# Optimization experiments

Measured on AMD Instinct MI355X. Metric: run time of the kernel, lower is better.

## Reference

```python
import jax, jax.numpy as jnp
import numpy as np

N_NODES = 50000
N_EDGES = 800000
IN_DIM = 128
HID_DIM = 64
N_HEADS = 4
OUT_DIM = 128
NEG_SLOPE = 0.2  # DGL GATConv default


def gat_conv(x, src, dst, W, attn_l, attn_r, bias, n_nodes):
    """DGL GATConv forward. x:[N,Fin], W:[Fin,H*D], attn_*:[H,D], bias:[H,D]. Returns [N,H,D]."""
    H, D = attn_l.shape
    h = (x @ W).reshape(n_nodes, H, D)              # [N,H,D]
    el = jnp.sum(h * attn_l[None], axis=-1)          # [N,H]
    er = jnp.sum(h * attn_r[None], axis=-1)          # [N,H]
    e = jax.nn.leaky_relu(el[src] + er[dst], NEG_SLOPE)  # [E,H]
    # edge softmax over incoming edges of each dst node (stable)
    m = jax.ops.segment_max(e, dst, num_segments=n_nodes)   # [N,H], -inf for empty
    ex = jnp.exp(e - m[dst])                                 # [E,H]
    denom = jax.ops.segment_sum(ex, dst, num_segments=n_nodes)  # [N,H]
    alpha = ex / denom[dst]                                  # [E,H]
    out = jax.ops.segment_sum(alpha[:, :, None] * h[src], dst, num_segments=n_nodes)
    return out + bias[None]                                  # [N,H,D]


def setup_inputs() -> dict:
    key = jax.random.key(0)
    ks = jax.random.split(key, 12)
    x = jax.random.normal(ks[0], (N_NODES, IN_DIM), dtype=jnp.float32)
    src = jax.random.randint(ks[1], (N_EDGES,), 0, N_NODES, dtype=jnp.int32)
    dst = jax.random.randint(ks[2], (N_EDGES,), 0, N_NODES, dtype=jnp.int32)
    s1 = 1.0 / np.sqrt(IN_DIM)
    s2 = 1.0 / np.sqrt(HID_DIM * N_HEADS)
    W1 = jax.random.normal(ks[3], (IN_DIM, N_HEADS * HID_DIM), dtype=jnp.float32) * s1
    al1 = jax.random.normal(ks[4], (N_HEADS, HID_DIM), dtype=jnp.float32) * 0.1
    ar1 = jax.random.normal(ks[5], (N_HEADS, HID_DIM), dtype=jnp.float32) * 0.1
    b1 = jnp.zeros((N_HEADS, HID_DIM), dtype=jnp.float32)
    W2 = jax.random.normal(ks[6], (N_HEADS * HID_DIM, OUT_DIM), dtype=jnp.float32) * s2
    al2 = jax.random.normal(ks[7], (1, OUT_DIM), dtype=jnp.float32) * 0.1
    ar2 = jax.random.normal(ks[8], (1, OUT_DIM), dtype=jnp.float32) * 0.1
    b2 = jnp.zeros((1, OUT_DIM), dtype=jnp.float32)
    return {"x": x, "src": src, "dst": dst, "W1": W1, "al1": al1, "ar1": ar1,
            "b1": b1, "W2": W2, "al2": al2, "ar2": ar2, "b2": b2}


def reference(x, src, dst, W1, al1, ar1, b1, W2, al2, ar2, b2):
    n = x.shape[0]
    h1 = gat_conv(x, src, dst, W1, al1, ar1, b1, n)          # [N,H,D]
    h1 = jax.nn.relu(h1).reshape(n, -1)                       # [N,H*D]
    h2 = gat_conv(h1, src, dst, W2, al2, ar2, b2, n)          # [N,1,OUT]
    return h2.reshape(n, -1)                                   # [N,OUT]
```

## Files before the change

kernel.cpp:

```cpp
#include <hip/hip_runtime.h>
#include <hip/hip_bf16.h>
#include <math.h>


#define NEG_SLOPE 0.2f
#define NB 256
#define CH 8192

typedef short short8 __attribute__((ext_vector_type(8)));
typedef float float4v __attribute__((ext_vector_type(4)));
typedef float float2v __attribute__((ext_vector_type(2)));

static __device__ __forceinline__ float lrelu(float v) {
    return v > 0.f ? v : NEG_SLOPE * v;
}

static __device__ __forceinline__ unsigned short f2bf(float f) {
    unsigned int u = __float_as_uint(f);
    u = (u + 0x7fffu + ((u >> 16) & 1u)) >> 16;
    return (unsigned short)u;
}
static __device__ __forceinline__ float bf2f(unsigned int lo16) {
    return __uint_as_float(lo16 << 16);
}

static __device__ __forceinline__ int bucket_of(int d, unsigned int M) {
    return (int)(((unsigned long long)(unsigned int)d * M) >> 32);
}

static __device__ __forceinline__ void pk_step(float2v& a00, float2v& a01,
                                               float2v& a10, float2v& a11,
                                               float2v& d0, float2v& d1,
                                               float4 w, unsigned int v) {
    float2v w01; w01[0] = w.x; w01[1] = w.y;
    float2v w23; w23[0] = w.z; w23[1] = w.w;
    float x0 = __uint_as_float(v << 16);
    float x1 = __uint_as_float(v & 0xffff0000u);
    float2v xx0 = {x0, x0};
    float2v xx1 = {x1, x1};
    asm("v_pk_fma_f32 %0, %1, %2, %0" : "+v"(a00) : "v"(w01), "v"(xx0));
    asm("v_pk_fma_f32 %0, %1, %2, %0" : "+v"(a01) : "v"(w23), "v"(xx0));
    asm("v_pk_fma_f32 %0, %1, %2, %0" : "+v"(a10) : "v"(w01), "v"(xx1));
    asm("v_pk_fma_f32 %0, %1, %2, %0" : "+v"(a11) : "v"(w23), "v"(xx1));
    asm("v_pk_add_f32 %0, %1, %0" : "+v"(d0) : "v"(w01));
    asm("v_pk_add_f32 %0, %1, %0" : "+v"(d1) : "v"(w23));
}


__global__ __launch_bounds__(256) void histbin_kernel(
        const int* __restrict__ dst, int* __restrict__ bcnt,
        int E, unsigned int M, int nblk,
        const float* __restrict__ W1, const float* __restrict__ al1,
        const float* __restrict__ ar1, const float* __restrict__ W2,
        const float* __restrict__ al2, const float* __restrict__ ar2,
        unsigned short* __restrict__ W1th, unsigned short* __restrict__ Qt1,
        unsigned short* __restrict__ Qt2, unsigned short* __restrict__ W2t) {
    int b = blockIdx.x;
    int tid = threadIdx.x;
    if (b < nblk) {
        __shared__ int lcnt[NB];
        lcnt[tid] = 0;
        __syncthreads();
        int e0 = b * CH;
        for (int i = tid; i < CH; i += 256) {
            int e = e0 + i;
            if (e < E) atomicAdd(&lcnt[bucket_of(dst[e], M)], 1);
        }
        __syncthreads();
        bcnt[b * NB + tid] = lcnt[tid];
        return;
    }
    int idx = (b - nblk) * 256 + tid;
    if (idx < 32768) {
        int h = idx >> 13;
        int r = idx & 8191;
        int d = r >> 7, k = r & 127;
        W1th[idx] = f2bf(W1[k * 256 + h * 64 + d]);
    } else if (idx < 34816) {
        int j = idx - 32768;
        int c = j >> 7, k = j & 127;
        float s = 0.f;
        if (c < 8) {
            int h = c & 3;
            const float* av = ((c < 4) ? al1 : ar1) + h * 64;
            const float* wrow = W1 + k * 256 + h * 64;
            #pragma unroll 8
            for (int d = 0; d < 64; ++d) s += wrow[d] * av[d];
        }
        Qt1[j] = f2bf(s);
    } else if (idx < 36864) {
        int j = idx - 34816;
        int c = j >> 7, k = j & 127;
        float s = (c == 0) ? al2[k] : (c == 1) ? ar2[k] : 0.f;
        Qt2[j] = f2bf(s);
    } else if (idx < 69632) {
        int j = idx - 36864;
        int m = j >> 8, k = j & 255;
        W2t[(size_t)m * 256 + k] = f2bf(W2[(size_t)k * 128 + m]);
    }
}


__global__ __launch_bounds__(256) void binscan_kernel(
        const int* __restrict__ bcnt, int* __restrict__ cur0,
        int* __restrict__ bucketStart, int nblk, int E) {
    __shared__ int s[NB];
    int t = threadIdx.x;
    int tot = 0;
    for (int blk = 0; blk < nblk; ++blk) tot += bcnt[blk * NB + t];
    s[t] = tot;
    __syncthreads();
    for (int off = 1; off < NB; off <<= 1) {
        int add = (t >= off) ? s[t - off] : 0;
        __syncthreads();
        s[t] += add;
        __syncthreads();
    }
    const int bs = s[t] - tot;
    bucketStart[t] = bs;
    if (t == NB - 1) bucketStart[NB] = E;
    int run = bs;
    for (int blk = 0; blk < nblk; ++blk) {
        int c = bcnt[blk * NB + t];
        cur0[blk * NB + t] = run;
        run += c;
    }
}


__global__ __launch_bounds__(256) void scatxdots_kernel(
        const int* __restrict__ src, const int* __restrict__ dst,
        const int* __restrict__ cur0,
        uint2* __restrict__ pairs, int E, unsigned int M, int nblk,
        const float* __restrict__ x, const unsigned short* __restrict__ Qt,
        unsigned short* __restrict__ xb,
        float* __restrict__ el, float* __restrict__ er, int N) {
    constexpr int KP = 136;
    __shared__ alignas(16) unsigned char smem[(64 + 16) * KP * 2];
    const int tid = threadIdx.x;
    if (blockIdx.x < (unsigned)nblk) {
        int* cur = (int*)smem;
        const int b = blockIdx.x;
        cur[tid] = cur0[b * NB + tid];
        __syncthreads();
        int e0 = b * CH;
        for (int i = tid; i < CH; i += 256) {
            int e = e0 + i;
            if (e < E) {
                int d = dst[e];
                int bk = bucket_of(d, M);
                int pos = atomicAdd(&cur[bk], 1);
                pairs[pos] = make_uint2((unsigned int)src[e], (unsigned int)d);
            }
        }
        return;
    }
    unsigned short* As = (unsigned short*)smem;
    unsigned short* Bs = As + 64 * KP;
    const int wid = tid >> 6, lane = tid & 63;
    const int r0 = (blockIdx.x - nblk) * 64;
    for (int ch = tid; ch < 64 * 16; ch += 256) {
        int row = ch >> 4, kc = ch & 15;
        int gr = r0 + row;
        short8 v = {};
        if (gr < N) {
            float4 a = *(const float4*)(x + (size_t)gr * 128 + kc * 8);
            float4 b = *(const float4*)(x + (size_t)gr * 128 + kc * 8 + 4);
            v[0] = (short)f2bf(a.x); v[1] = (short)f2bf(a.y);
            v[2] = (short)f2bf(a.z); v[3] = (short)f2bf(a.w);
            v[4] = (short)f2bf(b.x); v[5] = (short)f2bf(b.y);
            v[6] = (short)f2bf(b.z); v[7] = (short)f2bf(b.w);
            *(short8*)(xb + (size_t)gr * 128 + kc * 8) = v;
        }
        *(short8*)(As + row * KP + kc * 8) = v;
    }
    {
        int row = tid >> 4, kc = tid & 15;
        *(short8*)(Bs + row * KP + kc * 8) = *(const short8*)(Qt + row * 128 + kc * 8);
    }
    __syncthreads();
    float4v acc = (float4v){0.f, 0.f, 0.f, 0.f};
    const int lr = lane & 15, lk = (lane >> 4) * 8;
    #pragma unroll
    for (int ks = 0; ks < 128; ks += 32) {
        short8 af = *(const short8*)(As + (wid * 16 + lr) * KP + ks + lk);
        short8 bf_ = *(const short8*)(Bs + lr * KP + ks + lk);
        acc = __builtin_amdgcn_mfma_f32_16x16x32_bf16(af, bf_, acc, 0, 0, 0);
    }
    const int rbase = r0 + wid * 16 + (lane >> 4) * 4;
    #pragma unroll
    for (int j = 0; j < 4; ++j) {
        int row = rbase + j;
        if (row < N) {
            if (lr < 4) el[(size_t)row * 4 + lr] = acc[j];
            else if (lr < 8) er[(size_t)row * 4 + (lr - 4)] = acc[j];
        }
    }
}


__global__ __launch_bounds__(256) void bucketcsr_kernel(
        const uint2* __restrict__ pairs, const int* __restrict__ bucketStart,
        int* __restrict__ row_start, int* __restrict__ srcs,
        int N, int npb, int E) {
    __shared__ int cnt[NB];
    __shared__ int sc[NB];
    int b = blockIdx.x;
    int tid = threadIdx.x;
    int nb0 = b * npb;
    int es = bucketStart[b], ee = bucketStart[b + 1];
    cnt[tid] = 0;
    __syncthreads();
    for (int i = es + tid; i < ee; i += 256) {
        uint2 p = pairs[i];
        atomicAdd(&cnt[(int)p.y - nb0], 1);
    }
    __syncthreads();
    int myc = cnt[tid];
    sc[tid] = myc;
    __syncthreads();
    for (int off = 1; off < NB; off <<= 1) {
        int add = (tid >= off) ? sc[tid - off] : 0;
        __syncthreads();
        sc[tid] += add;
        __syncthreads();
    }
    int excl = sc[tid] - myc;
    int n = nb0 + tid;
    if (n < N && tid < npb) row_start[n] = es + excl;
    if (b == gridDim.x - 1 && tid == 0) row_start[N] = E;
    cnt[tid] = es + excl;
    __syncthreads();
    for (int i = es + tid; i < ee; i += 256) {
        uint2 p = pairs[i];
        int pos = atomicAdd(&cnt[(int)p.y - nb0], 1);
        srcs[pos] = (int)p.x;
    }
}


__global__ __launch_bounds__(256) void agg1x_kernel(const unsigned short* __restrict__ xb,
                            const float* __restrict__ el, const float* __restrict__ er,
                            const int* __restrict__ srcs, const int* __restrict__ row_start,
                            unsigned short* __restrict__ A1, int N) {
    __shared__ int   s_tbl[4][64];
    __shared__ float a_tbl[4][64][4];
    const int wslot = threadIdx.x >> 6;
    const int lane = threadIdx.x & 63;
    const int n = (blockIdx.x * 256 + threadIdx.x) >> 6;
    if (n >= N) return;
    const int rs = row_start[n];
    const int re = row_start[n + 1];

    float2v accP[2][2];
    accP[0][0] = (float2v){0.f, 0.f}; accP[0][1] = (float2v){0.f, 0.f};
    accP[1][0] = (float2v){0.f, 0.f}; accP[1][1] = (float2v){0.f, 0.f};
    float2v dP[2];
    dP[0] = (float2v){0.f, 0.f}; dP[1] = (float2v){0.f, 0.f};

    if (re > rs) {
        const float4 ern = *(const float4*)(er + (size_t)n * 4);
        for (int base = rs; base < re; base += 64) {
            const int cnt = (re - base) < 64 ? (re - base) : 64;
            asm volatile("s_waitcnt lgkmcnt(0)" ::: "memory");
            if (lane < cnt) {
                int sv = srcs[base + lane];
                float4 ev = *(const float4*)(el + (size_t)sv * 4);
                float4 av;
                av.x = __expf(lrelu(ev.x + ern.x));
                av.y = __expf(lrelu(ev.y + ern.y));
                av.z = __expf(lrelu(ev.z + ern.z));
                av.w = __expf(lrelu(ev.w + ern.w));
                s_tbl[wslot][lane] = sv;
                *(float4*)&a_tbl[wslot][lane][0] = av;
            }
            asm volatile("s_waitcnt lgkmcnt(0)" ::: "memory");
            int i = 0;
            for (; i + 4 <= cnt; i += 4) {
                int s0 = s_tbl[wslot][i],     s1 = s_tbl[wslot][i + 1];
                int s2 = s_tbl[wslot][i + 2], s3 = s_tbl[wslot][i + 3];
                float4 w0 = *(const float4*)&a_tbl[wslot][i][0];
                float4 w1 = *(const float4*)&a_tbl[wslot][i + 1][0];
                float4 w2 = *(const float4*)&a_tbl[wslot][i + 2][0];
                float4 w3 = *(const float4*)&a_tbl[wslot][i + 3][0];
                unsigned int v0 = *(const unsigned int*)(xb + (size_t)s0 * 128 + lane * 2);
                unsigned int v1 = *(const unsigned int*)(xb + (size_t)s1 * 128 + lane * 2);
                unsigned int v2 = *(const unsigned int*)(xb + (size_t)s2 * 128 + lane * 2);
                unsigned int v3 = *(const unsigned int*)(xb + (size_t)s3 * 128 + lane * 2);
                pk_step(accP[0][0], accP[0][1], accP[1][0], accP[1][1], dP[0], dP[1], w0, v0);
                pk_step(accP[0][0], accP[0][1], accP[1][0], accP[1][1], dP[0], dP[1], w1, v1);
                pk_step(accP[0][0], accP[0][1], accP[1][0], accP[1][1], dP[0], dP[1], w2, v2);
                pk_step(accP[0][0], accP[0][1], accP[1][0], accP[1][1], dP[0], dP[1], w3, v3);
            }
            for (; i < cnt; ++i) {
                int s0 = s_tbl[wslot][i];
                float4 w = *(const float4*)&a_tbl[wslot][i][0];
                unsigned int v = *(const unsigned int*)(xb + (size_t)s0 * 128 + lane * 2);
                pk_step(accP[0][0], accP[0][1], accP[1][0], accP[1][1], dP[0], dP[1], w, v);
            }
        }
        float i0 = 1.f / dP[0][0], i1 = 1.f / dP[0][1];
        float i2 = 1.f / dP[1][0], i3 = 1.f / dP[1][1];
        accP[0][0][0] *= i0; accP[1][0][0] *= i0;
        accP[0][0][1] *= i1; accP[1][0][1] *= i1;
        accP[0][1][0] *= i2; accP[1][1][0] *= i2;
        accP[0][1][1] *= i3; accP[1][1][1] *= i3;
    }
    unsigned int pk;
    pk = (unsigned int)f2bf(accP[0][0][0]) | ((unsigned int)f2bf(accP[1][0][0]) << 16);
    *(unsigned int*)(A1 + (size_t)n * 512 + 0 * 128 + lane * 2) = pk;
    pk = (unsigned int)f2bf(accP[0][0][1]) | ((unsigned int)f2bf(accP[1][0][1]) << 16);
    *(unsigned int*)(A1 + (size_t)n * 512 + 1 * 128 + lane * 2) = pk;
    pk = (unsigned int)f2bf(accP[0][1][0]) | ((unsigned int)f2bf(accP[1][1][0]) << 16);
    *(unsigned int*)(A1 + (size_t)n * 512 + 2 * 128 + lane * 2) = pk;
    pk = (unsigned int)f2bf(accP[0][1][1]) | ((unsigned int)f2bf(accP[1][1][1]) << 16);
    *(unsigned int*)(A1 + (size_t)n * 512 + 3 * 128 + lane * 2) = pk;
}


__global__ __launch_bounds__(256) void l2fused_kernel(
        const unsigned short* __restrict__ A1,
        const unsigned short* __restrict__ W1th,
        const float* __restrict__ b1,
        const unsigned short* __restrict__ W2t,
        const unsigned short* __restrict__ Qt2,
        unsigned short* __restrict__ h2b,
        float* __restrict__ el2, float* __restrict__ er2,
        int N) {
    constexpr int KP = 136;
    constexpr int PP = 72;
    __shared__ unsigned short As[64 * KP];
    __shared__ unsigned short Bs1[64 * KP];
    __shared__ unsigned short Bs2[128 * PP];
    __shared__ unsigned short Ps[64 * PP];
    __shared__ unsigned short Qs[16 * KP];
    const int tid = threadIdx.x;
    const int wid = tid >> 6, lane = tid & 63;
    const int lr = lane & 15, lk = (lane >> 4) * 8;
    const int r0 = blockIdx.x * 64;

    {
        int row = tid >> 4, kc = tid & 15;
        *(short8*)(Qs + row * KP + kc * 8) = *(const short8*)(Qt2 + row * 128 + kc * 8);
    }

    float4v acc2[8];
    #pragma unroll
    for (int cf = 0; cf < 8; ++cf) acc2[cf] = (float4v){0.f, 0.f, 0.f, 0.f};

    for (int h = 0; h < 4; ++h) {
        __syncthreads();
        for (int ch = tid; ch < 1024; ch += 256) {
            int row = ch >> 4, kc = ch & 15;
            int gr = r0 + row;
            short8 v = {};
            if (gr < N) v = *(const short8*)(A1 + (size_t)gr * 512 + h * 128 + kc * 8);
            *(short8*)(As + row * KP + kc * 8) = v;
        }
        for (int ch = tid; ch < 1024; ch += 256) {
            int row = ch >> 4, kc = ch & 15;
            *(short8*)(Bs1 + row * KP + kc * 8) =
                *(const short8*)(W1th + (size_t)h * 8192 + row * 128 + kc * 8);
        }
        for (int ch = tid; ch < 1024; ch += 256) {
            int m = ch >> 3, kc = ch & 7;
            *(short8*)(Bs2 + m * PP + kc * 8) =
                *(const short8*)(W2t + (size_t)m * 256 + h * 64 + kc * 8);
        }
        __syncthreads();

        float4v p[4];
        #pragma unroll
        for (int cf = 0; cf < 4; ++cf) p[cf] = (float4v){0.f, 0.f, 0.f, 0.f};
        #pragma unroll
        for (int ks = 0; ks < 128; ks += 32) {
            short8 af = *(const short8*)(As + (wid * 16 + lr) * KP + ks + lk);
            #pragma unroll
            for (int cf = 0; cf < 4; ++cf) {
                short8 bfr = *(const short8*)(Bs1 + (cf * 16 + lr) * KP + ks + lk);
                p[cf] = __builtin_amdgcn_mfma_f32_16x16x32_bf16(af, bfr, p[cf], 0, 0, 0);
            }
        }
        const int prow = wid * 16 + (lane >> 4) * 4;
        #pragma unroll
        for (int cf = 0; cf < 4; ++cf) {
            float bias = b1[h * 64 + cf * 16 + lr];
            #pragma unroll
            for (int j = 0; j < 4; ++j)
                Ps[(prow + j) * PP + cf * 16 + lr] = f2bf(fmaxf(p[cf][j] + bias, 0.f));
        }
        __syncthreads();

        #pragma unroll
        for (int ks2 = 0; ks2 < 64; ks2 += 32) {
            short8 af2 = *(const short8*)(Ps + (wid * 16 + lr) * PP + ks2 + lk);
            #pragma unroll
            for (int cf = 0; cf < 8; ++cf) {
                short8 bf2 = *(const short8*)(Bs2 + (cf * 16 + lr) * PP + ks2 + lk);
                acc2[cf] = __builtin_amdgcn_mfma_f32_16x16x32_bf16(af2, bf2, acc2[cf], 0, 0, 0);
            }
        }
    }

    const int prow = wid * 16 + (lane >> 4) * 4;
    #pragma unroll
    for (int cf = 0; cf < 8; ++cf) {
        int col = cf * 16 + lr;
        #pragma unroll
        for (int j = 0; j < 4; ++j) {
            unsigned short hv = f2bf(acc2[cf][j]);
            int row = prow + j;
            if (r0 + row < N) h2b[(size_t)(r0 + row) * 128 + col] = hv;
            As[row * KP + col] = hv;
        }
    }
    __syncthreads();
    float4v dd = (float4v){0.f, 0.f, 0.f, 0.f};
    #pragma unroll
    for (int ks = 0; ks < 128; ks += 32) {
        short8 af = *(const short8*)(As + (wid * 16 + lr) * KP + ks + lk);
        short8 bq = *(const short8*)(Qs + lr * KP + ks + lk);
        dd = __builtin_amdgcn_mfma_f32_16x16x32_bf16(af, bq, dd, 0, 0, 0);
    }
    #pragma unroll
    for (int j = 0; j < 4; ++j) {
        int row = r0 + prow + j;
        if (row < N) {
            if (lr == 0) el2[row] = dd[j];
            else if (lr == 1) er2[row] = dd[j];
        }
    }
}


__global__ __launch_bounds__(256) void agg2_kernel(const unsigned short* __restrict__ hb,
                           const float* __restrict__ el, const float* __restrict__ er,
                           const int* __restrict__ srcs, const int* __restrict__ row_start,
                           const float* __restrict__ bias, float* __restrict__ out, int N) {
    __shared__ uint2 t_tbl[4][64];
    const int wslot = threadIdx.x >> 6;
    const int lane = threadIdx.x & 63;
    const int n = (blockIdx.x * 256 + threadIdx.x) >> 6;
    if (n >= N) return;
    const int rs = row_start[n];
    const int re = row_start[n + 1];

    float acc0 = 0.f, acc1 = 0.f, d = 0.f;

    if (re > rs) {
        const float ern = er[n];
        for (int base = rs; base < re; base += 64) {
            const int cnt = (re - base) < 64 ? (re - base) : 64;
            asm volatile("s_waitcnt lgkmcnt(0)" ::: "memory");
            if (lane < cnt) {
                int sv = srcs[base + lane];
                float a = __expf(lrelu(el[sv] + ern));
                t_tbl[wslot][lane] = make_uint2((unsigned int)sv, __float_as_uint(a));
            }
            asm volatile("s_waitcnt lgkmcnt(0)" ::: "memory");
            int i = 0;
            for (; i + 4 <= cnt; i += 4) {
                uint2 t0 = t_tbl[wslot][i],     t1 = t_tbl[wslot][i + 1];
                uint2 t2 = t_tbl[wslot][i + 2], t3 = t_tbl[wslot][i + 3];
                float w0 = __uint_as_float(t0.y), w1 = __uint_as_float(t1.y);
                float w2 = __uint_as_float(t2.y), w3 = __uint_as_float(t3.y);
                unsigned int v0 = *(const unsigned int*)(hb + (size_t)t0.x * 128 + lane * 2);
                unsigned int v1 = *(const unsigned int*)(hb + (size_t)t1.x * 128 + lane * 2);
                unsigned int v2 = *(const unsigned int*)(hb + (size_t)t2.x * 128 + lane * 2);
                unsigned int v3 = *(const unsigned int*)(hb + (size_t)t3.x * 128 + lane * 2);
                d += w0 + w1 + w2 + w3;
                acc0 += w0 * bf2f(v0 & 0xffffu) + w1 * bf2f(v1 & 0xffffu) +
                        w2 * bf2f(v2 & 0xffffu) + w3 * bf2f(v3 & 0xffffu);
                acc1 += w0 * bf2f(v0 >> 16) + w1 * bf2f(v1 >> 16) +
                        w2 * bf2f(v2 >> 16) + w3 * bf2f(v3 >> 16);
            }
            for (; i < cnt; ++i) {
                uint2 t = t_tbl[wslot][i];
                float w = __uint_as_float(t.y);
                unsigned int v = *(const unsigned int*)(hb + (size_t)t.x * 128 + lane * 2);
                d += w;
                acc0 += w * bf2f(v & 0xffffu);
                acc1 += w * bf2f(v >> 16);
            }
        }
        float invd = 1.f / d;
        acc0 *= invd; acc1 *= invd;
    }
    float o0 = acc0 + bias[lane * 2];
    float o1 = acc1 + bias[lane * 2 + 1];
    *(float2*)(out + (size_t)n * 128 + lane * 2) = make_float2(o0, o1);
}


extern "C" void kernel_launch(void* const* d_in, const int* in_sizes, int n_in,
                              void* d_out, int out_size, void* d_ws, size_t ws_size,
                              hipStream_t stream) {
    const float* x   = (const float*)d_in[0];
    const int*   src = (const int*)d_in[1];
    const int*   dst = (const int*)d_in[2];
    const float* W1  = (const float*)d_in[3];
    const float* al1 = (const float*)d_in[4];
    const float* ar1 = (const float*)d_in[5];
    const float* b1  = (const float*)d_in[6];
    const float* W2  = (const float*)d_in[7];
    const float* al2 = (const float*)d_in[8];
    const float* ar2 = (const float*)d_in[9];
    const float* b2  = (const float*)d_in[10];
    float* out = (float*)d_out;

    const int N = in_sizes[0] / 128;
    const int E = in_sizes[1];
    const int npb = (N + NB - 1) / NB;
    const unsigned int M =
        (unsigned int)(((1ULL << 32) + npb - 1) / (unsigned long long)npb);
    const int nblk_e = (E + CH - 1) / CH;

    char* ws = (char*)d_ws;
    size_t oXB   = 0;
    size_t oA1   = oXB + (size_t)N * 128 * 2;
    size_t oH2   = oA1 + (size_t)N * 512 * 2;
    size_t oW1th = oH2 + (size_t)N * 128 * 2;
    size_t oQt1  = oW1th + 32768 * 2;
    size_t oQt2  = oQt1 + 2048 * 2;
    size_t oW2t  = oQt2 + 2048 * 2;
    size_t oEl1  = oW2t + 32768 * 2;
    size_t oEr1  = oEl1 + (size_t)N * 4 * 4;
    size_t oEl2  = oEr1 + (size_t)N * 4 * 4;
    size_t oEr2  = oEl2 + (size_t)N * 4;
    size_t oRow  = oEr2 + (size_t)N * 4;
    size_t oBcnt = oRow + (((size_t)(N + 1) * 4 + 15) & ~(size_t)15);
    size_t oCur0 = oBcnt + (size_t)nblk_e * NB * 4;
    size_t oBkS  = oCur0 + (size_t)nblk_e * NB * 4;
    size_t oPair = (oBkS + (NB + 1) * 4 + 15) & ~(size_t)15;
    size_t oSrcs = oPair + (size_t)E * 8;

    unsigned short* xb   = (unsigned short*)(ws + oXB);
    unsigned short* A1   = (unsigned short*)(ws + oA1);
    unsigned short* h2b  = (unsigned short*)(ws + oH2);
    unsigned short* w1th = (unsigned short*)(ws + oW1th);
    unsigned short* qt1  = (unsigned short*)(ws + oQt1);
    unsigned short* qt2  = (unsigned short*)(ws + oQt2);
    unsigned short* w2t  = (unsigned short*)(ws + oW2t);
    float* el1 = (float*)(ws + oEl1);
    float* er1 = (float*)(ws + oEr1);
    float* el2 = (float*)(ws + oEl2);
    float* er2 = (float*)(ws + oEr2);
    int*   row_start   = (int*)(ws + oRow);
    int*   bcnt        = (int*)(ws + oBcnt);
    int*   cur0        = (int*)(ws + oCur0);
    int*   bucketStart = (int*)(ws + oBkS);
    uint2* pairs       = (uint2*)(ws + oPair);
    int*   srcs        = (int*)(ws + oSrcs);

    const int nrowb = (N + 63) / 64;
    const int nwaveb = (N + 3) / 4;

    histbin_kernel<<<nblk_e + 272, 256, 0, stream>>>(
        dst, bcnt, E, M, nblk_e, W1, al1, ar1, W2, al2, ar2, w1th, qt1, qt2, w2t);

    binscan_kernel<<<1, 256, 0, stream>>>(bcnt, cur0, bucketStart, nblk_e, E);

    scatxdots_kernel<<<nblk_e + nrowb, 256, 0, stream>>>(
        src, dst, cur0, pairs, E, M, nblk_e,
        x, qt1, xb, el1, er1, N);

    bucketcsr_kernel<<<NB, 256, 0, stream>>>(pairs, bucketStart, row_start, srcs, N, npb, E);

    agg1x_kernel<<<nwaveb, 256, 0, stream>>>(xb, el1, er1, srcs, row_start, A1, N);

    l2fused_kernel<<<nrowb, 256, 0, stream>>>(A1, w1th, b1, w2t, qt2, h2b, el2, er2, N);

    agg2_kernel<<<nwaveb, 256, 0, stream>>>(h2b, el2, er2, srcs, row_start, b2, out, N);
}
```

Before: 192.7 us.

## Load MFMA operands directly from global memory in fused layer-2 kernel

The fused layer-2 projection kernel no longer stages the A1 tile, the W1 head slice, the W2 slice and the Qt2 matrix in shared memory. Each wave now reads its MFMA fragments straight from global memory (weights are expected to hit in cache), and a single shared buffer is reused for the intermediate P tile and the final output tile. This cuts LDS use from about 57KB to 17KB, which should raise occupancy, and removes the staging copies and their barriers. In exchange, weight fragments are re-read from global or L2 by every wave, and the global loads are less coalesced.

```diff
diff --git a/kernel.cpp b/kernel.cpp
--- a/kernel.cpp
+++ b/kernel.cpp
@@ -327,82 +327,59 @@
         unsigned short* __restrict__ h2b,
         float* __restrict__ el2, float* __restrict__ er2,
         int N) {
+    constexpr int PP = 72;
     constexpr int KP = 136;
-    constexpr int PP = 72;
-    __shared__ unsigned short As[64 * KP];
-    __shared__ unsigned short Bs1[64 * KP];
-    __shared__ unsigned short Bs2[128 * PP];
-    __shared__ unsigned short Ps[64 * PP];
-    __shared__ unsigned short Qs[16 * KP];
+    __shared__ unsigned short Sh[64 * KP];
     const int tid = threadIdx.x;
     const int wid = tid >> 6, lane = tid & 63;
     const int lr = lane & 15, lk = (lane >> 4) * 8;
     const int r0 = blockIdx.x * 64;
-
-    {
-        int row = tid >> 4, kc = tid & 15;
-        *(short8*)(Qs + row * KP + kc * 8) = *(const short8*)(Qt2 + row * 128 + kc * 8);
-    }
+    const int arow = r0 + wid * 16 + lr;
+    const bool arok = arow < N;
+    const int prow = wid * 16 + (lane >> 4) * 4;
 
     float4v acc2[8];
     #pragma unroll
     for (int cf = 0; cf < 8; ++cf) acc2[cf] = (float4v){0.f, 0.f, 0.f, 0.f};
 
     for (int h = 0; h < 4; ++h) {
-        __syncthreads();
-        for (int ch = tid; ch < 1024; ch += 256) {
-            int row = ch >> 4, kc = ch & 15;
-            int gr = r0 + row;
-            short8 v = {};
-            if (gr < N) v = *(const short8*)(A1 + (size_t)gr * 512 + h * 128 + kc * 8);
-            *(short8*)(As + row * KP + kc * 8) = v;
-        }
-        for (int ch = tid; ch < 1024; ch += 256) {
-            int row = ch >> 4, kc = ch & 15;
-            *(short8*)(Bs1 + row * KP + kc * 8) =
-                *(const short8*)(W1th + (size_t)h * 8192 + row * 128 + kc * 8);
-        }
-        for (int ch = tid; ch < 1024; ch += 256) {
-            int m = ch >> 3, kc = ch & 7;
-            *(short8*)(Bs2 + m * PP + kc * 8) =
-                *(const short8*)(W2t + (size_t)m * 256 + h * 64 + kc * 8);
-        }
-        __syncthreads();
-
         float4v p[4];
         #pragma unroll
         for (int cf = 0; cf < 4; ++cf) p[cf] = (float4v){0.f, 0.f, 0.f, 0.f};
+        const unsigned short* aptr = A1 + (size_t)arow * 512 + h * 128 + lk;
+        const unsigned short* w1p  = W1th + h * 8192 + lr * 128 + lk;
         #pragma unroll
         for (int ks = 0; ks < 128; ks += 32) {
-            short8 af = *(const short8*)(As + (wid * 16 + lr) * KP + ks + lk);
+            short8 af = {};
+            if (arok) af = *(const short8*)(aptr + ks);
             #pragma unroll
             for (int cf = 0; cf < 4; ++cf) {
-                short8 bfr = *(const short8*)(Bs1 + (cf * 16 + lr) * KP + ks + lk);
+                short8 bfr = *(const short8*)(w1p + cf * 2048 + ks);
                 p[cf] = __builtin_amdgcn_mfma_f32_16x16x32_bf16(af, bfr, p[cf], 0, 0, 0);
             }
         }
-        const int prow = wid * 16 + (lane >> 4) * 4;
+        __syncthreads();
         #pragma unroll
         for (int cf = 0; cf < 4; ++cf) {
             float bias = b1[h * 64 + cf * 16 + lr];
             #pragma unroll
             for (int j = 0; j < 4; ++j)
-                Ps[(prow + j) * PP + cf * 16 + lr] = f2bf(fmaxf(p[cf][j] + bias, 0.f));
-        }
-        __syncthreads();
-
+                Sh[(prow + j) * PP + cf * 16 + lr] = f2bf(fmaxf(p[cf][j] + bias, 0.f));
+        }
+        __syncthreads();
+        const unsigned short* w2p = W2t + (size_t)lr * 256 + h * 64 + lk;
         #pragma unroll
         for (int ks2 = 0; ks2 < 64; ks2 += 32) {
-            short8 af2 = *(const short8*)(Ps + (wid * 16 + lr) * PP + ks2 + lk);
+            short8 af2 = *(const short8*)(Sh + (wid * 16 + lr) * PP + ks2 + lk);
             #pragma unroll
             for (int cf = 0; cf < 8; ++cf) {
-                short8 bf2 = *(const short8*)(Bs2 + (cf * 16 + lr) * PP + ks2 + lk);
+                short8 bf2 = *(const short8*)(w2p + cf * 4096 + ks2);
                 acc2[cf] = __builtin_amdgcn_mfma_f32_16x16x32_bf16(af2, bf2, acc2[cf], 0, 0, 0);
             }
         }
     }
 
-    const int prow = wid * 16 + (lane >> 4) * 4;
+    __syncthreads();
     #pragma unroll
     for (int cf = 0; cf < 8; ++cf) {
         int col = cf * 16 + lr;
@@ -411,15 +388,16 @@
             unsigned short hv = f2bf(acc2[cf][j]);
             int row = prow + j;
             if (r0 + row < N) h2b[(size_t)(r0 + row) * 128 + col] = hv;
-            As[row * KP + col] = hv;
+            Sh[row * KP + col] = hv;
         }
     }
     __syncthreads();
     float4v dd = (float4v){0.f, 0.f, 0.f, 0.f};
+    const unsigned short* qp = Qt2 + lr * 128 + lk;
     #pragma unroll
     for (int ks = 0; ks < 128; ks += 32) {
-        short8 af = *(const short8*)(As + (wid * 16 + lr) * KP + ks + lk);
-        short8 bq = *(const short8*)(Qs + lr * KP + ks + lk);
+        short8 af = *(const short8*)(Sh + (wid * 16 + lr) * KP + ks + lk);
+        short8 bq = *(const short8*)(qp + ks);
         dd = __builtin_amdgcn_mfma_f32_16x16x32_bf16(af, bq, dd, 0, 0, 0);
     }
     #pragma unroll
```

Result: slower. 219.4 us (+13.9%).
